# Optimization experiments

Hardware: AMD Instinct MI355X
Metric: run time of the kernel (lower is better)

Reference implementation:

```python
import jax, jax.numpy as jnp
import numpy as np

N_HEADS = 16
HEAD_SIZE = 64
N_EMBD = N_HEADS * HEAD_SIZE  # 1024
B, T = 4, 2048


def setup_inputs() -> dict:
    key = jax.random.key(0)
    kx, kq, kk, kv, kp = jax.random.split(key, 5)
    s = 1.0 / np.sqrt(N_EMBD)
    return {
        "x": jax.random.normal(kx, (B, T, N_EMBD), dtype=jnp.float32),
        "Wq": jax.random.normal(kq, (N_EMBD, N_HEADS * HEAD_SIZE), dtype=jnp.float32) * s,
        "Wk": jax.random.normal(kk, (N_EMBD, N_HEADS * HEAD_SIZE), dtype=jnp.float32) * s,
        "Wv": jax.random.normal(kv, (N_EMBD, N_HEADS * HEAD_SIZE), dtype=jnp.float32) * s,
        "Wp": jax.random.normal(kp, (N_HEADS * HEAD_SIZE, N_EMBD), dtype=jnp.float32) * s,
    }


def reference(x, Wq, Wk, Wv, Wp):
    Bb, Tt, C = x.shape
    H, hs = N_HEADS, HEAD_SIZE
    # QKV projections (no bias), split heads: (B, H, T, hs)
    q = (x @ Wq).reshape(Bb, Tt, H, hs).transpose(0, 2, 1, 3)
    k = (x @ Wk).reshape(Bb, Tt, H, hs).transpose(0, 2, 1, 3)
    v = (x @ Wv).reshape(Bb, Tt, H, hs).transpose(0, 2, 1, 3)
    scores = jnp.einsum("bhqd,bhkd->bhqk", q, k) / np.sqrt(hs).astype(np.float32)
    causal = jnp.tril(jnp.ones((Tt, Tt), dtype=bool))
    scores = jnp.where(causal, scores, -jnp.inf)
    attn = jax.nn.softmax(scores, axis=-1)  # dropout p=0 -> identity
    o = jnp.einsum("bhqk,bhkd->bhqd", attn, v)  # (B, H, T, hs)
    # Faithfully replicate torch's view/transpose/view sequence:
    o = o.reshape(Bb, Tt, H * hs)          # raw reshape of (B,H,T,hs) buffer
    o = jnp.swapaxes(o, 1, 2)               # (B, H*hs, T)
    o = o.reshape(Bb, Tt, H * hs)           # contiguous().view
    return o @ Wp
```

## Files before the change

### kernel.cpp

```cpp
#include <hip/hip_runtime.h>

typedef unsigned short ush;
typedef unsigned int u32;
typedef __attribute__((ext_vector_type(4))) float f32x4;
typedef __attribute__((ext_vector_type(8))) short short8;
typedef __attribute__((ext_vector_type(8))) ush ushx8;
typedef __attribute__((ext_vector_type(4))) ush ushx4;

#define GAS __attribute__((address_space(1)))
#define LAS __attribute__((address_space(3)))

__device__ __forceinline__ void gl_lds16(const void* g, void* l) {
  __builtin_amdgcn_global_load_lds((const GAS void*)g, (LAS void*)l, 16, 0, 0);
}

__device__ __forceinline__ ush f2bf(float f) {
  union { float f; unsigned int u; } x; x.f = f;
  unsigned int r = x.u + 0x7fffu + ((x.u >> 16) & 1u);
  return (ush)(r >> 16);
}
__device__ __forceinline__ u32 fbits(float f) {
  union { float f; u32 u; } x; x.f = f; return x.u;
}

#define NEG_BIG (-1.0e4f)
#define SCL 0.18033688f

__global__ __launch_bounds__(256) void k_convert_x(
    const float* __restrict__ X, ush* __restrict__ Xb) {
  int idx = blockIdx.x * 256 + threadIdx.x;
  int base = idx * 8;
  f32x4 a = *(const f32x4*)(X + base);
  f32x4 b = *(const f32x4*)(X + base + 4);
  ushx8 o;
#pragma unroll
  for (int q = 0; q < 4; ++q) { o[q] = f2bf(a[q]); o[4 + q] = f2bf(b[q]); }
  *(ushx8*)(Xb + base) = o;
}

__global__ __launch_bounds__(256) void k_transpose_w(
    const float* __restrict__ W0, const float* __restrict__ W1,
    const float* __restrict__ W2, const float* __restrict__ W3,
    ush* __restrict__ Wt) {
  __shared__ ush Ts[64][72];
  const int z = blockIdx.z;
  const float* W = (z == 0) ? W0 : (z == 1) ? W1 : (z == 2) ? W2 : W3;
  ush* Ot = Wt + (size_t)z * 1048576;
  const int k0 = blockIdx.x * 64, n0 = blockIdx.y * 64;
  const int rr = threadIdx.x >> 4, cc = threadIdx.x & 15;
#pragma unroll
  for (int i = 0; i < 4; ++i) {
    int row = i * 16 + rr;
    f32x4 v = *(const f32x4*)(W + (size_t)(k0 + row) * 1024 + n0 + cc * 4);
#pragma unroll
    for (int q = 0; q < 4; ++q) Ts[row][cc * 4 + q] = f2bf(v[q]);
  }
  __syncthreads();
#pragma unroll
  for (int i = 0; i < 4; ++i) {
    int n = i * 16 + rr;
    ushx4 o;
#pragma unroll
    for (int q = 0; q < 4; ++q) o[q] = Ts[cc * 4 + q][n];
    *(ushx4*)(Ot + (size_t)(n0 + n) * 1024 + k0 + cc * 4) = o;
  }
}

__global__ __launch_bounds__(256) void k_gemm_qkv(
    const ush* __restrict__ X, const ush* __restrict__ Wt, ush* __restrict__ QKV) {
  __shared__ __align__(16) ush sm[16384];
  ush* As = sm;
  ush* Bs = sm + 8192;
  const int tid = threadIdx.x;
  const int w = tid >> 6, l = tid & 63, lr = l & 15, lg = l >> 4;
  const int mt = blockIdx.x, nt = blockIdx.y;
  const int which = nt >> 3, n0 = (nt & 7) * 128;
  const ush* Ag = X + (size_t)mt * 128 * 1024;
  const ush* Bg = Wt + (size_t)which * 1048576 + (size_t)n0 * 1024;
  const int wr = (w >> 1) * 64, wc = (w & 1) * 64;
  f32x4 acc[4][4] = {};
  for (int k0 = 0; k0 < 1024; k0 += 64) {
#pragma unroll
    for (int it = 0; it < 4; ++it) {
      int c = it * 256 + tid;
      int row = c >> 3, c8 = (c & 7) * 8;
      gl_lds16(Ag + (size_t)row * 1024 + k0 + c8, As + c * 8);
      gl_lds16(Bg + (size_t)row * 1024 + k0 + c8, Bs + c * 8);
    }
    asm volatile("s_waitcnt vmcnt(0)" ::: "memory");
    __syncthreads();
    short8 fa[2][4], fb[2][4];
#pragma unroll
    for (int s = 0; s < 2; ++s)
#pragma unroll
      for (int i = 0; i < 4; ++i) {
        fa[s][i] = *(const short8*)(As + (wr + i * 16 + lr) * 64 + s * 32 + lg * 8);
        fb[s][i] = *(const short8*)(Bs + (wc + i * 16 + lr) * 64 + s * 32 + lg * 8);
      }
#pragma unroll
    for (int s = 0; s < 2; ++s)
#pragma unroll
      for (int mi = 0; mi < 4; ++mi)
#pragma unroll
        for (int ni = 0; ni < 4; ++ni)
          acc[mi][ni] = __builtin_amdgcn_mfma_f32_16x16x32_bf16(fa[s][mi], fb[s][ni], acc[mi][ni], 0, 0, 0);
    __syncthreads();
  }
  ush* Ct = sm;
#pragma unroll
  for (int mi = 0; mi < 4; ++mi)
#pragma unroll
    for (int ni = 0; ni < 4; ++ni)
#pragma unroll
      for (int j = 0; j < 4; ++j)
        Ct[(wr + mi * 16 + lg * 4 + j) * 128 + wc + ni * 16 + lr] = f2bf(acc[mi][ni][j]);
  __syncthreads();
  ush* Om = QKV + (size_t)which * 8388608;
  const int m0 = mt * 128, b = m0 >> 11, t0 = m0 & 2047, h0 = n0 >> 6;
#pragma unroll
  for (int it = 0; it < 8; ++it) {
    int c = it * 256 + tid;
    int half = c >> 10;
    int cc = c & 1023;
    int r = cc >> 3;
    int c8 = (cc & 7) * 8;
    ushx8 v = *(const ushx8*)(Ct + r * 128 + half * 64 + c8);
    *(ushx8*)(Om + ((size_t)(b * 16 + h0 + half) * 2048 + t0 + r) * 64 + c8) = v;
  }
}

__global__ __launch_bounds__(256) void k_attn(
    const ush* __restrict__ Q, const ush* __restrict__ K,
    const ush* __restrict__ V, ush* __restrict__ O) {
  __shared__ __align__(16) ush Ks[4096];
  __shared__ __align__(16) ush Vt[4096];
  __shared__ __align__(16) ush Pl[8][1024];
  const int qta = blockIdx.x;
  const int qtb = 31 - qta;
  const int bh = blockIdx.y;
  const size_t hb = (size_t)bh * (2048 * 64);
  const ush* Qh = Q + hb;
  const ush* Kh = K + hb;
  const ush* Vh = V + hb;
  const int tid = threadIdx.x, w = tid >> 6, l = tid & 63, lr = l & 15, lg = l >> 4;
  const int q0a = qta * 64 + w * 16, q0b = qtb * 64 + w * 16;

  short8 qfa[2], qfb[2];
#pragma unroll
  for (int s = 0; s < 2; ++s) {
    qfa[s] = *(const short8*)(Qh + (size_t)(q0a + lr) * 64 + s * 32 + lg * 8);
    qfb[s] = *(const short8*)(Qh + (size_t)(q0b + lr) * 64 + s * 32 + lg * 8);
  }
  f32x4 acca[4] = {}, accb[4] = {};
  float la[4] = {0.f, 0.f, 0.f, 0.f}, lb[4] = {0.f, 0.f, 0.f, 0.f};

  ushx8 kreg[2], vreg[2];
  auto loadKV = [&](int c) {
#pragma unroll
    for (int it = 0; it < 2; ++it) {
      int ch = it * 256 + tid;
      int row = ch >> 3, cb = (ch & 7) * 8;
      kreg[it] = *(const ushx8*)(Kh + ((size_t)c * 64 + row) * 64 + cb);
      vreg[it] = *(const ushx8*)(Vh + ((size_t)c * 64 + row) * 64 + cb);
    }
  };
  auto stage = [&]() {
#pragma unroll
    for (int it = 0; it < 2; ++it) {
      int ch = it * 256 + tid;
      int row = ch >> 3, g = ch & 7;
      *(ushx8*)(Ks + row * 64 + ((g ^ (row & 7)) << 3)) = kreg[it];
#pragma unroll
      for (int jj = 0; jj < 8; ++jj) {
        int d = g * 8 + jj;
        int key = (jj + g) & 7;
        Vt[d * 64 + (row ^ (key << 3))] = vreg[it][jj];
      }
    }
  };

  auto ctile = [&](const short8* qf, f32x4* acc, float* lrow, bool diag, ush* PlW) {
    f32x4 sf[4] = {};
#pragma unroll
    for (int s = 0; s < 2; ++s)
#pragma unroll
      for (int f = 0; f < 4; ++f) {
        int kv = f * 16 + lr;
        short8 kf = *(const short8*)(Ks + kv * 64 + (((s * 4 + lg) ^ (kv & 7)) << 3));
        sf[f] = __builtin_amdgcn_mfma_f32_16x16x32_bf16(qf[s], kf, sf[f], 0, 0, 0);
      }
#pragma unroll
    for (int f = 0; f < 4; ++f)
#pragma unroll
      for (int j = 0; j < 4; ++j) {
        float vv = sf[f][j] * SCL;
        if (diag && (f * 16 + lr) > (w * 16 + lg * 4 + j)) vv = NEG_BIG;
        sf[f][j] = __builtin_amdgcn_exp2f(vv);
      }
#pragma unroll
    for (int j = 0; j < 4; ++j)
      lrow[j] += (sf[0][j] + sf[1][j]) + (sf[2][j] + sf[3][j]);
#pragma unroll
    for (int f = 0; f < 4; ++f)
#pragma unroll
      for (int j = 0; j < 4; ++j) {
        int q = lg * 4 + j;
        PlW[q * 64 + ((f * 16 + lr) ^ ((q & 7) << 3))] = (ush)(fbits(sf[f][j]) >> 16);
      }
#pragma unroll
    for (int s = 0; s < 2; ++s) {
      short8 pf = *(const short8*)(PlW + lr * 64 + (((s * 4 + lg) ^ (lr & 7)) << 3));
#pragma unroll
      for (int db = 0; db < 4; ++db) {
        int dv = db * 16 + lr;
        int keyv = ((dv & 7) + (dv >> 3)) & 7;
        short8 vf = *(const short8*)(Vt + dv * 64 + (((s * 4 + lg) ^ keyv) << 3));
        acc[db] = __builtin_amdgcn_mfma_f32_16x16x32_bf16(pf, vf, acc[db], 0, 0, 0);
      }
    }
  };

  loadKV(0);
  for (int c = 0; c <= qtb; ++c) {
    __syncthreads();
    stage();
    __syncthreads();
    if (c < qtb) loadKV(c + 1);
    if (c <= qta) ctile(qfa, acca, la, c == qta, Pl[w]);
    ctile(qfb, accb, lb, c == qtb, Pl[4 + w]);
  }

#pragma unroll
  for (int msk = 1; msk <= 8; msk <<= 1)
#pragma unroll
    for (int j = 0; j < 4; ++j) {
      la[j] += __shfl_xor(la[j], msk);
      lb[j] += __shfl_xor(lb[j], msk);
    }
  float ia[4], ib[4];
#pragma unroll
  for (int j = 0; j < 4; ++j) {
    ia[j] = __builtin_amdgcn_rcpf(la[j]);
    ib[j] = __builtin_amdgcn_rcpf(lb[j]);
  }
  ush* Oh = O + hb;
#pragma unroll
  for (int db = 0; db < 4; ++db)
#pragma unroll
    for (int j = 0; j < 4; ++j) {
      Oh[(size_t)(q0a + lg * 4 + j) * 64 + db * 16 + lr] = f2bf(acca[db][j] * ia[j]);
      Oh[(size_t)(q0b + lg * 4 + j) * 64 + db * 16 + lr] = f2bf(accb[db][j] * ib[j]);
    }
}

__global__ __launch_bounds__(256) void k_gather(const ush* __restrict__ Ob, ush* __restrict__ Mb) {
  __shared__ ush Ls[2][128][68];
  const int jh = blockIdx.x, tau = blockIdx.y, b = blockIdx.z;
  const int tid = threadIdx.x;
#pragma unroll
  for (int it = 0; it < 8; ++it) {
    int c = it * 256 + tid;
    int r = c >> 3, d8 = (c & 7) * 8;
    int esel = r >> 7, jlow = r & 127;
    ushx8 v = *(const ushx8*)(Ob +
        ((size_t)(b * 16 + jh + esel * 8) * 2048 + jlow * 16 + tau) * 64 + d8);
    *(ushx8*)(&Ls[esel][jlow][d8]) = v;
  }
  __syncthreads();
  const int wv = tid >> 6, l = tid & 63;
  const int e = wv >> 1, jhalf = wv & 1, d = l;
  ush* Mrow = Mb + (size_t)b * 2097152 +
              (size_t)(128 * tau + 2 * d + e) * 1024 + jh * 128 + jhalf * 64;
#pragma unroll
  for (int ch = 0; ch < 8; ++ch) {
    ushx8 v;
#pragma unroll
    for (int k = 0; k < 8; ++k) v[k] = Ls[e][jhalf * 64 + ch * 8 + k][d];
    *(ushx8*)(Mrow + ch * 8) = v;
  }
}

__global__ __launch_bounds__(256) void k_gemm_out(
    const ush* __restrict__ A, const ush* __restrict__ Bt, float* __restrict__ Out) {
  __shared__ __align__(16) ush sm[16384];
  ush* As = sm;
  ush* Bs = sm + 8192;
  const int tid = threadIdx.x;
  const int w = tid >> 6, l = tid & 63, lr = l & 15, lg = l >> 4;
  const int mt = blockIdx.x, nt = blockIdx.y;
  const int n0 = nt * 128;
  const ush* Ag = A + (size_t)mt * 128 * 1024;
  const ush* Bg = Bt + (size_t)n0 * 1024;
  const int wr = (w >> 1) * 64, wc = (w & 1) * 64;
  f32x4 acc[4][4] = {};
  for (int k0 = 0; k0 < 1024; k0 += 64) {
#pragma unroll
    for (int it = 0; it < 4; ++it) {
      int c = it * 256 + tid;
      int row = c >> 3, c8 = (c & 7) * 8;
      gl_lds16(Ag + (size_t)row * 1024 + k0 + c8, As + c * 8);
      gl_lds16(Bg + (size_t)row * 1024 + k0 + c8, Bs + c * 8);
    }
    asm volatile("s_waitcnt vmcnt(0)" ::: "memory");
    __syncthreads();
    short8 fa[2][4], fb[2][4];
#pragma unroll
    for (int s = 0; s < 2; ++s)
#pragma unroll
      for (int i = 0; i < 4; ++i) {
        fa[s][i] = *(const short8*)(As + (wr + i * 16 + lr) * 64 + s * 32 + lg * 8);
        fb[s][i] = *(const short8*)(Bs + (wc + i * 16 + lr) * 64 + s * 32 + lg * 8);
      }
#pragma unroll
    for (int s = 0; s < 2; ++s)
#pragma unroll
      for (int mi = 0; mi < 4; ++mi)
#pragma unroll
        for (int ni = 0; ni < 4; ++ni)
          acc[mi][ni] = __builtin_amdgcn_mfma_f32_16x16x32_bf16(fa[s][mi], fb[s][ni], acc[mi][ni], 0, 0, 0);
    __syncthreads();
  }
  const int m0 = mt * 128;
#pragma unroll
  for (int mi = 0; mi < 4; ++mi)
#pragma unroll
    for (int ni = 0; ni < 4; ++ni)
#pragma unroll
      for (int j = 0; j < 4; ++j)
        Out[(size_t)(m0 + wr + mi * 16 + lg * 4 + j) * 1024 + n0 + wc + ni * 16 + lr] =
            acc[mi][ni][j];
}

extern "C" void kernel_launch(void* const* d_in, const int* in_sizes, int n_in,
                              void* d_out, int out_size, void* d_ws, size_t ws_size,
                              hipStream_t stream) {
  const float* x  = (const float*)d_in[0];
  const float* wq = (const float*)d_in[1];
  const float* wk = (const float*)d_in[2];
  const float* wv = (const float*)d_in[3];
  const float* wp = (const float*)d_in[4];
  float* out = (float*)d_out;
  char* ws = (char*)d_ws;
  ush* xb  = (ush*)ws;
  ush* wt  = (ush*)(ws + 16777216);
  ush* qkv = (ush*)(ws + 25165824);
  ush* ob  = qkv;
  ush* mb  = xb;

  k_convert_x<<<dim3(4096), 256, 0, stream>>>(x, xb);
  k_transpose_w<<<dim3(16, 16, 4), 256, 0, stream>>>(wq, wk, wv, wp, wt);
  k_gemm_qkv<<<dim3(64, 24), 256, 0, stream>>>(xb, wt, qkv);
  k_attn<<<dim3(16, 64), 256, 0, stream>>>(qkv, qkv + 8388608, qkv + 16777216, ob);
  k_gather<<<dim3(8, 16, 4), 256, 0, stream>>>(ob, mb);
  k_gemm_out<<<dim3(64, 8), 256, 0, stream>>>(mb, wt + 3145728, out);
}
```

Before: 219.3 us.

## Pre-transpose V and double-buffer K/V via direct global-to-LDS loads in attention

Adds a separate kernel that transposes V into a per-head (d, T) layout so the attention kernel can stage V tiles with 16-byte direct global-to-LDS loads instead of scalar transposing writes. K and V tiles are double-buffered in LDS, with the next chunk issued before computing the current one, which removes the register staging and one barrier per step. Block indices are also remapped so neighbouring blocks share heads, which may improve L2 locality. The cost is an extra kernel launch with a full pass over V, plus doubled LDS use that may reduce occupancy.

Result: no change. 218.4 us (-0.4%).

```diff
diff --git a/kernel.cpp b/kernel.cpp
--- a/kernel.cpp
+++ b/kernel.cpp
@@ -129,19 +129,47 @@
   }
 }
 
+__global__ __launch_bounds__(256) void k_transpose_v(
+    const ush* __restrict__ V, ush* __restrict__ Vt) {
+  __shared__ ush Ts[64][66];
+  const int tt = blockIdx.x, bh = blockIdx.y;
+  const ush* Vh = V + (size_t)bh * 131072 + tt * 4096;
+  ush* Oh = Vt + (size_t)bh * 131072 + tt * 64;
+  const int tid = threadIdx.x;
+#pragma unroll
+  for (int it = 0; it < 2; ++it) {
+    int idx = it * 256 + tid;
+    int row = idx >> 3, c8 = (idx & 7) * 8;
+    ushx8 v = *(const ushx8*)(Vh + row * 64 + c8);
+#pragma unroll
+    for (int k2 = 0; k2 < 8; ++k2) Ts[row][c8 + k2] = v[k2];
+  }
+  __syncthreads();
+#pragma unroll
+  for (int it = 0; it < 2; ++it) {
+    int idx = it * 256 + tid;
+    int d = idx >> 3, c8 = (idx & 7) * 8;
+    ushx8 o;
+#pragma unroll
+    for (int k2 = 0; k2 < 8; ++k2) o[k2] = Ts[c8 + k2][d];
+    *(ushx8*)(Oh + (size_t)d * 2048 + c8) = o;
+  }
+}
+
 __global__ __launch_bounds__(256) void k_attn(
     const ush* __restrict__ Q, const ush* __restrict__ K,
-    const ush* __restrict__ V, ush* __restrict__ O) {
-  __shared__ __align__(16) ush Ks[4096];
-  __shared__ __align__(16) ush Vt[4096];
+    const ush* __restrict__ Vg, ush* __restrict__ O) {
+  __shared__ __align__(16) ush Ks[2][4096];
+  __shared__ __align__(16) ush Vs[2][4096];
   __shared__ __align__(16) ush Pl[8][1024];
-  const int qta = blockIdx.x;
+  const int lid = blockIdx.x + 16 * blockIdx.y;
+  const int qta = (lid >> 3) & 15;
+  const int bh  = ((lid >> 7) << 3) | (lid & 7);
   const int qtb = 31 - qta;
-  const int bh = blockIdx.y;
   const size_t hb = (size_t)bh * (2048 * 64);
   const ush* Qh = Q + hb;
   const ush* Kh = K + hb;
-  const ush* Vh = V + hb;
+  const ush* Vh = Vg + hb;
   const int tid = threadIdx.x, w = tid >> 6, l = tid & 63, lr = l & 15, lg = l >> 4;
   const int q0a = qta * 64 + w * 16, q0b = qtb * 64 + w * 16;
 
@@ -154,39 +182,33 @@
   f32x4 acca[4] = {}, accb[4] = {};
   float la[4] = {0.f, 0.f, 0.f, 0.f}, lb[4] = {0.f, 0.f, 0.f, 0.f};
 
-  ushx8 kreg[2], vreg[2];
-  auto loadKV = [&](int c) {
+  int koff[2], voff[2];
+#pragma unroll
+  for (int it = 0; it < 2; ++it) {
+    int ch = it * 256 + tid;
+    int r = ch >> 3, g = ch & 7;
+    koff[it] = r * 64 + ((g ^ (r & 7)) << 3);
+    int keyv = ((r & 7) + (r >> 3)) & 7;
+    voff[it] = r * 2048 + ((g ^ keyv) << 3);
+  }
+  auto issueStage = [&](int c, int buf) {
 #pragma unroll
     for (int it = 0; it < 2; ++it) {
       int ch = it * 256 + tid;
-      int row = ch >> 3, cb = (ch & 7) * 8;
-      kreg[it] = *(const ushx8*)(Kh + ((size_t)c * 64 + row) * 64 + cb);
-      vreg[it] = *(const ushx8*)(Vh + ((size_t)c * 64 + row) * 64 + cb);
+      gl_lds16(Kh + (size_t)c * 4096 + koff[it], &Ks[buf][ch * 8]);
+      gl_lds16(Vh + c * 64 + voff[it], &Vs[buf][ch * 8]);
     }
   };
-  auto stage = [&]() {
-#pragma unroll
-    for (int it = 0; it < 2; ++it) {
-      int ch = it * 256 + tid;
-      int row = ch >> 3, g = ch & 7;
-      *(ushx8*)(Ks + row * 64 + ((g ^ (row & 7)) << 3)) = kreg[it];
-#pragma unroll
-      for (int jj = 0; jj < 8; ++jj) {
-        int d = g * 8 + jj;
-        int key = (jj + g) & 7;
-        Vt[d * 64 + (row ^ (key << 3))] = vreg[it][jj];
-      }
-    }
-  };
-
-  auto ctile = [&](const short8* qf, f32x4* acc, float* lrow, bool diag, ush* PlW) {
+
+  auto ctile = [&](const ush* Kc, const ush* Vc, const short8* qf,
+                   f32x4* acc, float* lrow, bool diag, ush* PlW) {
     f32x4 sf[4] = {};
 #pragma unroll
     for (int s = 0; s < 2; ++s)
 #pragma unroll
       for (int f = 0; f < 4; ++f) {
         int kv = f * 16 + lr;
-        short8 kf = *(const short8*)(Ks + kv * 64 + (((s * 4 + lg) ^ (kv & 7)) << 3));
+        short8 kf = *(const short8*)(Kc + kv * 64 + (((s * 4 + lg) ^ (kv & 7)) << 3));
         sf[f] = __builtin_amdgcn_mfma_f32_16x16x32_bf16(qf[s], kf, sf[f], 0, 0, 0);
       }
 #pragma unroll
@@ -214,20 +236,24 @@
       for (int db = 0; db < 4; ++db) {
         int dv = db * 16 + lr;
         int keyv = ((dv & 7) + (dv >> 3)) & 7;
-        short8 vf = *(const short8*)(Vt + dv * 64 + (((s * 4 + lg) ^ keyv) << 3));
+        short8 vf = *(const short8*)(Vc + dv * 64 + (((s * 4 + lg) ^ keyv) << 3));
         acc[db] = __builtin_amdgcn_mfma_f32_16x16x32_bf16(pf, vf, acc[db], 0, 0, 0);
       }
     }
   };
 
-  loadKV(0);
+  issueStage(0, 0);
+  int cur = 0;
   for (int c = 0; c <= qtb; ++c) {
-    __syncthreads();
-    stage();
-    __syncthreads();
-    if (c < qtb) loadKV(c + 1);
-    if (c <= qta) ctile(qfa, acca, la, c == qta, Pl[w]);
-    ctile(qfb, accb, lb, c == qtb, Pl[4 + w]);
+    asm volatile("s_waitcnt vmcnt(0)" ::: "memory");
+    __syncthreads();
+    if (c < qtb) issueStage(c + 1, cur ^ 1);
+    const ush* Kc = Ks[cur];
+    const ush* Vc = Vs[cur];
+    if (c <= qta) ctile(Kc, Vc, qfa, acca, la, c == qta, Pl[w]);
+    ctile(Kc, Vc, qfb, accb, lb, c == qtb, Pl[4 + w]);
+    __syncthreads();
+    cur ^= 1;
   }
 
 #pragma unroll
@@ -344,13 +370,15 @@
   ush* xb  = (ush*)ws;
   ush* wt  = (ush*)(ws + 16777216);
   ush* qkv = (ush*)(ws + 25165824);
+  ush* vtg = xb;
   ush* ob  = qkv;
   ush* mb  = xb;
 
   k_convert_x<<<dim3(4096), 256, 0, stream>>>(x, xb);
   k_transpose_w<<<dim3(16, 16, 4), 256, 0, stream>>>(wq, wk, wv, wp, wt);
   k_gemm_qkv<<<dim3(64, 24), 256, 0, stream>>>(xb, wt, qkv);
-  k_attn<<<dim3(16, 64), 256, 0, stream>>>(qkv, qkv + 8388608, qkv + 16777216, ob);
+  k_transpose_v<<<dim3(32, 64), 256, 0, stream>>>(qkv + 16777216, vtg);
+  k_attn<<<dim3(16, 64), 256, 0, stream>>>(qkv, qkv + 8388608, vtg, ob);
   k_gather<<<dim3(8, 16, 4), 256, 0, stream>>>(ob, mb);
   k_gemm_out<<<dim3(64, 8), 256, 0, stream>>>(mb, wt + 3145728, out);
 }
```
